# Performance work log

Measured on AMD Instinct MI355X. Metric: run time of the kernel, lower is better.

Reference implementation:

```python
import jax, jax.numpy as jnp
import numpy as np

EPS = 1e-6

def rms_norm(x, w):
    # x: (..., hd), w: (hd,)
    norm = jax.lax.rsqrt(jnp.mean(x * x, axis=-1, keepdims=True) + EPS)
    return x * norm * w

def rotate_half(x):
    x1, x2 = jnp.split(x, 2, axis=-1)
    return jnp.concatenate((-x2, x1), axis=-1)

def setup_inputs() -> dict:
    key = jax.random.key(0)
    ks = jax.random.split(key, 5)
    B, L, C, H = 8, 1024, 1024, 16
    hd = C // H
    x = jax.random.normal(ks[0], (B, L, C), dtype=jnp.float32)
    # RoPE tables (realistic: derived from angles; any broadcastable table works)
    pos = jnp.arange(L, dtype=jnp.float32)[:, None]
    inv_freq = 1.0 / (10000.0 ** (jnp.arange(0, hd, 2, dtype=jnp.float32) / hd))
    ang = pos * inv_freq[None, :]              # (L, hd/2)
    ang = jnp.concatenate([ang, ang], axis=-1) # (L, hd)
    cos = jnp.cos(ang)
    sin = jnp.sin(ang)
    w_qkv = jax.random.normal(ks[1], (3 * C, C), dtype=jnp.float32) * (C ** -0.5)
    w_proj = jax.random.normal(ks[2], (C, C), dtype=jnp.float32) * (C ** -0.5)
    q_norm_w = jnp.ones((hd,), dtype=jnp.float32)
    k_norm_w = jnp.ones((hd,), dtype=jnp.float32)
    return {"x": x, "cos": cos, "sin": sin, "w_qkv": w_qkv, "w_proj": w_proj,
            "q_norm_w": q_norm_w, "k_norm_w": k_norm_w}

def reference(x, cos, sin, w_qkv, w_proj, q_norm_w, k_norm_w):
    B, L, C = x.shape
    H = 16
    hd = C // H
    # qkv: torch Linear(bias=False) -> x @ W^T, W: (3C, C)
    qkv = jnp.einsum('blc,dc->bld', x, w_qkv)             # (B, L, 3C)
    qkv = qkv.reshape(B, L, 3, H, hd).transpose(2, 0, 3, 1, 4)  # (3, B, H, L, hd)
    q, k, v = qkv[0], qkv[1], qkv[2]
    q = rms_norm(q, q_norm_w)
    k = rms_norm(k, k_norm_w)
    # RoPE: cos/sin (L, hd) broadcast over (B, H, L, hd)
    q = q * cos + rotate_half(q) * sin
    k = k * cos + rotate_half(k) * sin
    scale = 1.0 / np.sqrt(hd).astype(np.float32)
    attn = jnp.einsum('bhqd,bhkd->bhqk', q, k) * scale    # (B, H, L, L)
    attn = jax.nn.softmax(attn, axis=-1)
    out = jnp.einsum('bhqk,bhkd->bhqd', attn, v)          # (B, H, L, hd)
    out = out.transpose(0, 2, 1, 3).reshape(B, L, C)
    return jnp.einsum('blc,dc->bld', out, w_proj)
```

## Files before the change

### kernel.cpp

```cpp
#include <hip/hip_runtime.h>
#include <hip/hip_bf16.h>
#include <stdint.h>

typedef uint16_t u16;
typedef uint32_t u32;
typedef __attribute__((ext_vector_type(8))) short bv8;
typedef __attribute__((ext_vector_type(4))) float f32x4;
typedef __attribute__((ext_vector_type(16))) float f32x16;
typedef __attribute__((ext_vector_type(2))) u32 u32x2;

#define MFMA(a,b,c)   __builtin_amdgcn_mfma_f32_16x16x32_bf16((a),(b),(c),0,0,0)
#define MFMA32(a,b,c) __builtin_amdgcn_mfma_f32_32x32x16_bf16((a),(b),(c),0,0,0)

__device__ __forceinline__ float bf2f(u16 v){ u32 x=(u32)v<<16; float f; __builtin_memcpy(&f,&x,4); return f; }
__device__ __forceinline__ u16 f2bf(float f){ u32 x; __builtin_memcpy(&x,&f,4); x += 0x7fffu + ((x>>16)&1u); return (u16)(x>>16); }
__device__ __forceinline__ u32 cvtpk_bf16(float lo, float hi){
  u32 r; asm("v_cvt_pk_bf16_f32 %0, %1, %2" : "=v"(r) : "v"(lo), "v"(hi)); return r;
}
__device__ __forceinline__ float exp2_fast(float x){
  float r; asm("v_exp_f32 %0, %1" : "=v"(r) : "v"(x)); return r;
}

__device__ __forceinline__ void gl_lds16(const u16* g, u16* l){
  __builtin_amdgcn_global_load_lds((const __attribute__((address_space(1))) u32*)g,
                                   (__attribute__((address_space(3))) u32*)l, 16, 0, 0);
}

__global__ __launch_bounds__(256) void cvt_bf16(const float* __restrict__ src, u16* __restrict__ dst, long n8){
  long i = (long)blockIdx.x*256 + threadIdx.x;
  long stride = (long)gridDim.x*256;
  for(; i<n8; i+=stride){
    f32x4 a = *(const f32x4*)(src + i*8);
    f32x4 b = *(const f32x4*)(src + i*8 + 4);
    bv8 o;
    #pragma unroll
    for(int j=0;j<4;j++) o[j]   = (short)f2bf(a[j]);
    #pragma unroll
    for(int j=0;j<4;j++) o[4+j] = (short)f2bf(b[j]);
    *(bv8*)(dst + i*8) = o;
  }
}

template<int MODE>
__global__ __launch_bounds__(256,2) void gemm_bt(const u16* __restrict__ A, const u16* __restrict__ B,
                                                 void* __restrict__ Cv, int M, int N, int K,
                                                 const float* __restrict__ cosT,
                                                 const float* __restrict__ sinT,
                                                 const float* __restrict__ qw,
                                                 const float* __restrict__ kw){
  __shared__ __align__(16) u16 As[128*64];
  __shared__ __align__(16) u16 Bs[128*64];
  int nwg = gridDim.x;
  int wg  = (int)blockIdx.x;
  wg = (wg & 7)*(nwg>>3) + (wg>>3);
  int nn = N>>7;
  int tm = wg/nn, tn = wg - tm*nn;
  int rowbase = tm<<7, colbase = tn<<7;
  int t = threadIdx.x, lane = t&63, w = t>>6;
  int g = lane>>4, q16 = lane&15;
  int wr = w>>1, wc = w&1;

  f32x4 z = {0.f,0.f,0.f,0.f};
  f32x4 acc[4][4];
  #pragma unroll
  for(int i=0;i<4;i++)
    #pragma unroll
    for(int j=0;j<4;j++) acc[i][j]=z;

  for(int k0=0;k0<K;k0+=64){
    __syncthreads();
    #pragma unroll
    for(int i=0;i<4;i++){
      int s = ((w<<2)+i)*64 + lane;
      int row = s>>3;
      int ksl = (s&7) ^ (row&7);
      gl_lds16(A + (size_t)(rowbase+row)*K + k0 + ksl*8, (u16*)As + ((w<<2)+i)*512);
      gl_lds16(B + (size_t)(colbase+row)*K + k0 + ksl*8, (u16*)Bs + ((w<<2)+i)*512);
    }
    __syncthreads();
    #pragma unroll
    for(int eks=0;eks<2;eks++){
      bv8 af[4], bfr[4];
      #pragma unroll
      for(int mi=0;mi<4;mi++){
        int row = (wr<<6)+(mi<<4)+q16;
        af[mi] = *(const bv8*)(As + row*64 + ((((eks<<2)|g) ^ (row&7))<<3));
      }
      #pragma unroll
      for(int ni=0;ni<4;ni++){
        int row = (wc<<6)+(ni<<4)+q16;
        bfr[ni] = *(const bv8*)(Bs + row*64 + ((((eks<<2)|g) ^ (row&7))<<3));
      }
      #pragma unroll
      for(int mi=0;mi<4;mi++)
        #pragma unroll
        for(int ni=0;ni<4;ni++)
          acc[mi][ni] = MFMA(af[mi], bfr[ni], acc[mi][ni]);
    }
  }

  if(MODE==2 && colbase < 2048){
    int s = colbase>>10;
    const float* wsel = s ? kw : qw;
    int ch = colbase + (wc<<6);
    float qsc = s ? 1.0f : 0.1803368801111437f;
    float wv[4];
    #pragma unroll
    for(int ni=0;ni<4;ni++) wv[ni] = wsel[(ni<<4)|q16];
    #pragma unroll
    for(int mi=0;mi<4;mi++){
      #pragma unroll
      for(int r=0;r<4;r++){
        int row = rowbase + (wr<<6)+(mi<<4)+(g<<2)+r;
        int l = row & 1023;
        float y[4];
        float ss = 0.f;
        #pragma unroll
        for(int ni=0;ni<4;ni++){ y[ni]=acc[mi][ni][r]; ss += y[ni]*y[ni]; }
        ss += __shfl_xor(ss,1,64); ss += __shfl_xor(ss,2,64);
        ss += __shfl_xor(ss,4,64); ss += __shfl_xor(ss,8,64);
        float nrm = rsqrtf(ss*(1.f/64.f) + 1e-6f);
        #pragma unroll
        for(int ni=0;ni<4;ni++) y[ni] *= nrm * wv[ni];
        u16* cp = (u16*)Cv + (size_t)row*N + ch;
        #pragma unroll
        for(int ni=0;ni<4;ni++){
          int d = (ni<<4)|q16;
          float rot = (ni<2) ? -y[ni+2] : y[ni-2];
          float o = (y[ni]*cosT[l*64+d] + rot*sinT[l*64+d]) * qsc;
          cp[d] = f2bf(o);
        }
      }
    }
    return;
  }

  #pragma unroll
  for(int mi=0;mi<4;mi++){
    #pragma unroll
    for(int ni=0;ni<4;ni++){
      int row = rowbase + (wr<<6) + (mi<<4) + (g<<2);
      int col = colbase + (wc<<6) + (ni<<4) + q16;
      if(MODE==1){
        float* cp = (float*)Cv + (size_t)row*N + col;
        #pragma unroll
        for(int r=0;r<4;r++) cp[(size_t)r*N] = acc[mi][ni][r];
      } else {
        u16* cp = (u16*)Cv + (size_t)row*N + col;
        #pragma unroll
        for(int r=0;r<4;r++) cp[(size_t)r*N] = f2bf(acc[mi][ni][r]);
      }
    }
  }
}

__global__ __launch_bounds__(512,1) void fattn(const u16* __restrict__ qkv, u16* __restrict__ Out){
  __shared__ __align__(16) u16 Ks0[128*64];
  __shared__ __align__(16) u16 Ks1[128*64];
  __shared__ __align__(16) u16 Vt[64*128];

  int t = threadIdx.x, lane = t&63, w = t>>6;
  int ql = lane&31, h = lane>>5;
  int nwg = gridDim.x;
  int bid = (int)blockIdx.x;
  bid = (bid & 7)*(nwg>>3) + (bid>>3);
  int bh = bid >> 2, qt = bid & 3;
  int b = bh >> 4, hd = bh & 15;
  const u16* base = qkv + (size_t)b*1024*3072;
  int Qb = (qt<<8) + (w<<5);

  bv8 qf[4];
  {
    const u16* qp = base + (size_t)(Qb+ql)*3072 + hd*64 + (h<<3);
    qf[0] = *(const bv8*)(qp);
    qf[1] = *(const bv8*)(qp+16);
    qf[2] = *(const bv8*)(qp+32);
    qf[3] = *(const bv8*)(qp+48);
  }
  f32x16 accO0, accO1;
  #pragma unroll
  for(int r=0;r<16;r++){ accO0[r]=0.f; accO1[r]=0.f; }
  float m_run = -1e30f, l_run = 0.f;

  bool vstage = (t < 256);
  int d0v = (t&7)<<3;
  int c4  = (t>>3)&31;
  int sV = c4>>1, halfV = c4&1, kvr = c4<<2;
  int d15b = (t&1)<<3;

  bv8 v0,v1,v2,v3;
  const u16* gV0 = base + (size_t)kvr*3072 + 2048 + hd*64 + d0v;

#define LDV(tl) if(vstage){ const u16* gV = gV0 + (size_t)(tl)*393216; \
    v0 = *(const bv8*)(gV);       v1 = *(const bv8*)(gV+3072); \
    v2 = *(const bv8*)(gV+6144);  v3 = *(const bv8*)(gV+9216); }

#define STV() if(vstage){ \
    _Pragma("unroll") \
    for(int i=0;i<8;i++){ \
      int d = d0v + i; \
      u32x2 val; \
      val.x = (u32)(u16)v0[i] | ((u32)(u16)v1[i]<<16); \
      val.y = (u32)(u16)v2[i] | ((u32)(u16)v3[i]<<16); \
      *(u32x2*)(Vt + d*128 + (((sV ^ (d15b+i))<<3) + (halfV<<2))) = val; \
    } }

#define KDMA(tl, buf) { \
    _Pragma("unroll") \
    for(int i=0;i<2;i++){ \
      int si = ((w<<1)+i)*64 + lane; \
      int row = si>>3; \
      int esl = (si&7) ^ (row&7); \
      gl_lds16(base + (size_t)(((tl)<<7)+row)*3072 + 1024 + hd*64 + esl*8, (buf) + ((w<<1)+i)*512); \
    } }

  KDMA(0, (u16*)Ks0);
  LDV(0);

  for(int tile=0; tile<8; ++tile){
    u16* kcur = (tile&1) ? (u16*)Ks1 : (u16*)Ks0;
    u16* knxt = (tile&1) ? (u16*)Ks0 : (u16*)Ks1;
    if(tile>0) __syncthreads();
    STV();
    __syncthreads();
    if(tile<7){
      KDMA(tile+1, knxt);
      LDV(tile+1);
    }

    #pragma unroll
    for(int sub=0; sub<2; ++sub){
      f32x16 s0, s1;
      #pragma unroll
      for(int r=0;r<16;r++){ s0[r]=0.f; s1[r]=0.f; }
      int rowA = (sub<<6) + ql;
      int rowB = rowA + 32;
      __builtin_amdgcn_s_setprio(1);
      #pragma unroll
      for(int s=0;s<4;s++){
        bv8 ka = *(const bv8*)(kcur + rowA*64 + ((((s<<1)|h) ^ (rowA&7))<<3));
        bv8 kb = *(const bv8*)(kcur + rowB*64 + ((((s<<1)|h) ^ (rowB&7))<<3));
        s0 = MFMA32(ka, qf[s], s0);
        s1 = MFMA32(kb, qf[s], s1);
      }
      __builtin_amdgcn_s_setprio(0);

      float rm = -1e30f;
      #pragma unroll
      for(int r=0;r<16;r++){ rm = fmaxf(rm, fmaxf(s0[r], s1[r])); }
      rm = fmaxf(rm, __shfl_xor(rm, 32, 64));
      if(__any(rm > m_run + 8.0f)){
        float mnew = fmaxf(m_run, rm);
        float fac = exp2_fast(m_run - mnew);
        m_run = mnew;
        l_run *= fac;
        #pragma unroll
        for(int r=0;r<16;r++){
          int qs = (r&3) + ((r>>2)<<3) + (h<<2);
          float fr = __shfl(fac, qs, 64);
          accO0[r] *= fr; accO1[r] *= fr;
        }
      }
      float ps = 0.f;
      #pragma unroll
      for(int r=0;r<16;r++){
        float p0 = exp2_fast(s0[r]-m_run); s0[r] = p0;
        float p1 = exp2_fast(s1[r]-m_run); s1[r] = p1;
        ps += p0 + p1;
      }
      ps += __shfl_xor(ps, 32, 64);
      l_run += ps;

      int dsw = ql & 15;
      #pragma unroll
      for(int tt=0; tt<4; ++tt){
        int b0 = (tt&1)<<1;
        float a0,a1,a2,a3,b4,b5,b6,b7;
        if(tt<2){ a0=s0[4*b0+0]; a1=s0[4*b0+1]; a2=s0[4*b0+2]; a3=s0[4*b0+3];
                  b4=s0[4*b0+4]; b5=s0[4*b0+5]; b6=s0[4*b0+6]; b7=s0[4*b0+7]; }
        else    { a0=s1[4*b0+0]; a1=s1[4*b0+1]; a2=s1[4*b0+2]; a3=s1[4*b0+3];
                  b4=s1[4*b0+4]; b5=s1[4*b0+5]; b6=s1[4*b0+6]; b7=s1[4*b0+7]; }
        u32 Wlo0 = cvtpk_bf16(a0,a1), Wlo1 = cvtpk_bf16(a2,a3);
        u32 Whi0 = cvtpk_bf16(b4,b5), Whi1 = cvtpk_bf16(b6,b7);
        u32 X0 = h ? Wlo0 : Whi0;
        u32 X1 = h ? Wlo1 : Whi1;
        u32 x0 = (u32)__shfl_xor((int)X0, 32, 64);
        u32 x1 = (u32)__shfl_xor((int)X1, 32, 64);
        union { u32 u[4]; bv8 v; } pf;
        pf.u[0] = h ? x0 : Wlo0;
        pf.u[1] = h ? x1 : Wlo1;
        pf.u[2] = h ? Whi0 : x0;
        pf.u[3] = h ? Whi1 : x1;
        int vslot = ((sub<<3)+(tt<<1)+h) ^ dsw;
        bv8 vf0 = *(const bv8*)(Vt + ql*128 + (vslot<<3));
        bv8 vf1 = *(const bv8*)(Vt + (32+ql)*128 + (vslot<<3));
        __builtin_amdgcn_s_setprio(1);
        accO0 = MFMA32(pf.v, vf0, accO0);
        accO1 = MFMA32(pf.v, vf1, accO1);
        __builtin_amdgcn_s_setprio(0);
      }
    }
  }
  float linv = 1.f/l_run;
  #pragma unroll
  for(int r=0;r<16;r++){
    int qs = (r&3) + ((r>>2)<<3) + (h<<2);
    float li = __shfl(linv, qs, 64);
    size_t o = (size_t)(b*1024 + Qb + qs)*1024 + hd*64 + ql;
    Out[o]      = f2bf(accO0[r]*li);
    Out[o + 32] = f2bf(accO1[r]*li);
  }
#undef LDV
#undef STV
#undef KDMA
}

extern "C" void kernel_launch(void* const* d_in, const int* in_sizes, int n_in,
                              void* d_out, int out_size, void* d_ws, size_t ws_size,
                              hipStream_t stream) {
  const float* x      = (const float*)d_in[0];
  const float* cosT   = (const float*)d_in[1];
  const float* sinT   = (const float*)d_in[2];
  const float* w_qkv  = (const float*)d_in[3];
  const float* w_proj = (const float*)d_in[4];
  const float* qw     = (const float*)d_in[5];
  const float* kw     = (const float*)d_in[6];
  float* out = (float*)d_out;

  u16* xb     = (u16*)d_ws;
  u16* wqkvb  = xb     + (size_t) 8388608;
  u16* wprojb = wqkvb  + (size_t) 3145728;
  u16* qkv    = wprojb + (size_t) 1048576;
  u16* attn   = xb;

  cvt_bf16<<<2048, 256, 0, stream>>>(x,      xb,     1048576);
  cvt_bf16<<<1536, 256, 0, stream>>>(w_qkv,  wqkvb,   393216);
  cvt_bf16<<< 512, 256, 0, stream>>>(w_proj, wprojb,  131072);

  gemm_bt<2><<<1536, 256, 0, stream>>>(xb, wqkvb, qkv, 8192, 3072, 1024,
                                       cosT, sinT, qw, kw);
  fattn   <<<512, 512, 0, stream>>>(qkv, attn);
  gemm_bt<1><<<512, 256, 0, stream>>>(attn, wprojb, out, 8192, 1024, 1024,
                                      nullptr, nullptr, nullptr, nullptr);
}
```

Measured before the change: 180.5 us.

## Double-buffer V in attention, compute row sums via MFMA, merge conversion kernels

```diff
diff --git a/kernel.cpp b/kernel.cpp
--- a/kernel.cpp
+++ b/kernel.cpp
@@ -20,18 +20,27 @@
 __device__ __forceinline__ float exp2_fast(float x){
   float r; asm("v_exp_f32 %0, %1" : "=v"(r) : "v"(x)); return r;
 }
+__device__ __forceinline__ float rcp_fast(float x){
+  float r; asm("v_rcp_f32 %0, %1" : "=v"(r) : "v"(x)); return r;
+}
 
 __device__ __forceinline__ void gl_lds16(const u16* g, u16* l){
   __builtin_amdgcn_global_load_lds((const __attribute__((address_space(1))) u32*)g,
                                    (__attribute__((address_space(3))) u32*)l, 16, 0, 0);
 }
 
-__global__ __launch_bounds__(256) void cvt_bf16(const float* __restrict__ src, u16* __restrict__ dst, long n8){
+__global__ __launch_bounds__(256) void cvt3(const float* __restrict__ x, const float* __restrict__ wq,
+                                            const float* __restrict__ wp, u16* __restrict__ dst){
+  const long NA = 1048576, NB = 393216, NC = 131072;
   long i = (long)blockIdx.x*256 + threadIdx.x;
   long stride = (long)gridDim.x*256;
-  for(; i<n8; i+=stride){
-    f32x4 a = *(const f32x4*)(src + i*8);
-    f32x4 b = *(const f32x4*)(src + i*8 + 4);
+  for(; i < NA+NB+NC; i += stride){
+    const float* s;
+    if(i < NA)            s = x  + i*8;
+    else if(i < NA+NB)    s = wq + (i-NA)*8;
+    else                  s = wp + (i-NA-NB)*8;
+    f32x4 a = *(const f32x4*)(s);
+    f32x4 b = *(const f32x4*)(s + 4);
     bv8 o;
     #pragma unroll
     for(int j=0;j<4;j++) o[j]   = (short)f2bf(a[j]);
@@ -157,7 +166,7 @@
 __global__ __launch_bounds__(512,1) void fattn(const u16* __restrict__ qkv, u16* __restrict__ Out){
   __shared__ __align__(16) u16 Ks0[128*64];
   __shared__ __align__(16) u16 Ks1[128*64];
-  __shared__ __align__(16) u16 Vt[64*128];
+  __shared__ __align__(16) u16 Vt[2][64*128];
 
   int t = threadIdx.x, lane = t&63, w = t>>6;
   int ql = lane&31, h = lane>>5;
@@ -177,10 +186,14 @@
     qf[2] = *(const bv8*)(qp+32);
     qf[3] = *(const bv8*)(qp+48);
   }
-  f32x16 accO0, accO1;
-  #pragma unroll
-  for(int r=0;r<16;r++){ accO0[r]=0.f; accO1[r]=0.f; }
-  float m_run = -1e30f, l_run = 0.f;
+  bv8 onesb;
+  #pragma unroll
+  for(int j=0;j<8;j++) onesb[j] = (short)0x3F80;
+
+  f32x16 accO0, accO1, accL;
+  #pragma unroll
+  for(int r=0;r<16;r++){ accO0[r]=0.f; accO1[r]=0.f; accL[r]=0.f; }
+  float m_run = -1e30f;
 
   bool vstage = (t < 256);
   int d0v = (t&7)<<3;
@@ -195,14 +208,14 @@
     v0 = *(const bv8*)(gV);       v1 = *(const bv8*)(gV+3072); \
     v2 = *(const bv8*)(gV+6144);  v3 = *(const bv8*)(gV+9216); }
 
-#define STV() if(vstage){ \
+#define STV(buf) if(vstage){ \
     _Pragma("unroll") \
     for(int i=0;i<8;i++){ \
       int d = d0v + i; \
       u32x2 val; \
       val.x = (u32)(u16)v0[i] | ((u32)(u16)v1[i]<<16); \
       val.y = (u32)(u16)v2[i] | ((u32)(u16)v3[i]<<16); \
-      *(u32x2*)(Vt + d*128 + (((sV ^ (d15b+i))<<3) + (halfV<<2))) = val; \
+      *(u32x2*)((buf) + d*128 + (((sV ^ (d15b+i))<<3) + (halfV<<2))) = val; \
     } }
 
 #define KDMA(tl, buf) { \
@@ -216,17 +229,20 @@
 
   KDMA(0, (u16*)Ks0);
   LDV(0);
+  STV(Vt[0]);
+  LDV(1);
 
   for(int tile=0; tile<8; ++tile){
     u16* kcur = (tile&1) ? (u16*)Ks1 : (u16*)Ks0;
     u16* knxt = (tile&1) ? (u16*)Ks0 : (u16*)Ks1;
-    if(tile>0) __syncthreads();
-    STV();
+    u16* vcur = Vt[tile&1];
+    u16* vnxt = Vt[(tile&1)^1];
     __syncthreads();
     if(tile<7){
       KDMA(tile+1, knxt);
-      LDV(tile+1);
-    }
+      STV(vnxt);
+    }
+    if(tile<6) LDV(tile+2);
 
     #pragma unroll
     for(int sub=0; sub<2; ++sub){
@@ -253,23 +269,18 @@
         float mnew = fmaxf(m_run, rm);
         float fac = exp2_fast(m_run - mnew);
         m_run = mnew;
-        l_run *= fac;
         #pragma unroll
         for(int r=0;r<16;r++){
           int qs = (r&3) + ((r>>2)<<3) + (h<<2);
           float fr = __shfl(fac, qs, 64);
-          accO0[r] *= fr; accO1[r] *= fr;
+          accO0[r] *= fr; accO1[r] *= fr; accL[r] *= fr;
         }
       }
-      float ps = 0.f;
       #pragma unroll
       for(int r=0;r<16;r++){
-        float p0 = exp2_fast(s0[r]-m_run); s0[r] = p0;
-        float p1 = exp2_fast(s1[r]-m_run); s1[r] = p1;
-        ps += p0 + p1;
-      }
-      ps += __shfl_xor(ps, 32, 64);
-      l_run += ps;
+        s0[r] = exp2_fast(s0[r]-m_run);
+        s1[r] = exp2_fast(s1[r]-m_run);
+      }
 
       int dsw = ql & 15;
       #pragma unroll
@@ -292,20 +303,20 @@
         pf.u[2] = h ? Whi0 : x0;
         pf.u[3] = h ? Whi1 : x1;
         int vslot = ((sub<<3)+(tt<<1)+h) ^ dsw;
-        bv8 vf0 = *(const bv8*)(Vt + ql*128 + (vslot<<3));
-        bv8 vf1 = *(const bv8*)(Vt + (32+ql)*128 + (vslot<<3));
+        bv8 vf0 = *(const bv8*)(vcur + ql*128 + (vslot<<3));
+        bv8 vf1 = *(const bv8*)(vcur + (32+ql)*128 + (vslot<<3));
         __builtin_amdgcn_s_setprio(1);
         accO0 = MFMA32(pf.v, vf0, accO0);
         accO1 = MFMA32(pf.v, vf1, accO1);
+        accL  = MFMA32(pf.v, onesb, accL);
         __builtin_amdgcn_s_setprio(0);
       }
     }
   }
-  float linv = 1.f/l_run;
   #pragma unroll
   for(int r=0;r<16;r++){
     int qs = (r&3) + ((r>>2)<<3) + (h<<2);
-    float li = __shfl(linv, qs, 64);
+    float li = rcp_fast(accL[r]);
     size_t o = (size_t)(b*1024 + Qb + qs)*1024 + hd*64 + ql;
     Out[o]      = f2bf(accO0[r]*li);
     Out[o + 32] = f2bf(accO1[r]*li);
@@ -333,9 +344,7 @@
   u16* qkv    = wprojb + (size_t) 1048576;
   u16* attn   = xb;
 
-  cvt_bf16<<<2048, 256, 0, stream>>>(x,      xb,     1048576);
-  cvt_bf16<<<1536, 256, 0, stream>>>(w_qkv,  wqkvb,   393216);
-  cvt_bf16<<< 512, 256, 0, stream>>>(w_proj, wprojb,  131072);
+  cvt3<<<3072, 256, 0, stream>>>(x, w_qkv, w_proj, xb);
 
   gemm_bt<2><<<1536, 256, 0, stream>>>(xb, wqkvb, qkv, 8192, 3072, 1024,
                                        cosT, sinT, qw, kw);
```

After: 174.7 us. 1.03x faster.
